# Kernel tuning notes

Measured on AMD Instinct MI355X. Metric: run time of the kernel, lower is better.

## Reference

```python
import jax, jax.numpy as jnp
import numpy as np

B, N, DIM = 1, 2048, 2048
H, KVH = 32, 4                 # query heads, kv heads
D = DIM // H                   # head_dim = 64
REP = H // KVH                 # queries per kv = 8
KV_DIM = D * KVH               # 256


def _rope_tables(n, d, base=10000.0):
    inv = 1.0 / (base ** (np.arange(0, d, 2, dtype=np.float32) / d))
    t = np.arange(n, dtype=np.float32)
    freqs = np.outer(t, inv)                      # [n, d/2]
    emb = np.concatenate([freqs, freqs], axis=-1)  # [n, d]
    return jnp.asarray(np.cos(emb)), jnp.asarray(np.sin(emb))


def setup_inputs() -> dict:
    key = jax.random.key(0)
    ks = jax.random.split(key, 5)
    s = 0.02
    cos, sin = _rope_tables(N, D)
    return {
        "x": jax.random.normal(ks[0], (B, N, DIM), jnp.float32),
        "Wq": jax.random.normal(ks[1], (DIM, DIM), jnp.float32) * s,
        "Wk": jax.random.normal(ks[2], (KV_DIM, DIM), jnp.float32) * s,
        "Wv": jax.random.normal(ks[3], (KV_DIM, DIM), jnp.float32) * s,
        "Wo": jax.random.normal(ks[4], (DIM, DIM), jnp.float32) * s,
        "cos": cos,
        "sin": sin,
    }


def _rotate_half(t):
    d2 = t.shape[-1] // 2
    return jnp.concatenate([-t[..., d2:], t[..., :d2]], axis=-1)


def reference(x, Wq, Wk, Wv, Wo, cos, sin):
    b, n, _ = x.shape
    # projections (nn.Linear: x @ W.T)
    q = (x @ Wq.T).reshape(b, n, H, D).transpose(0, 2, 1, 3)     # b h n d
    k = (x @ Wk.T).reshape(b, n, KVH, D).transpose(0, 2, 1, 3)   # b g n d
    v = (x @ Wv.T).reshape(b, n, KVH, D).transpose(0, 2, 1, 3)
    # RoPE
    c = cos[None, None, :, :]
    s = sin[None, None, :, :]
    q = q * c + _rotate_half(q) * s
    k = k * c + _rotate_half(k) * s
    # expand KV heads (repeat_interleave over head dim)
    k = jnp.repeat(k, REP, axis=1)   # b h n d
    v = jnp.repeat(v, REP, axis=1)
    # causal attention with materialized scores (faithful to source)
    scale = 1.0 / jnp.sqrt(jnp.asarray(D, x.dtype))
    scores = jnp.einsum('bhld,bhsd->bhls', q, k) * scale
    causal = jnp.tril(jnp.ones((n, n), bool))
    scores = jnp.where(causal[None, None], scores, jnp.asarray(-jnp.inf, x.dtype))
    attn = jax.nn.softmax(scores, axis=-1)
    y = jnp.einsum('bhls,bhsd->bhld', attn, v)       # b h n d
    y = y.transpose(0, 2, 1, 3).reshape(b, n, DIM)   # b n (h d)
    return y @ Wo.T
```

## Files before the change

kernel.cpp:

```cpp
#include <hip/hip_runtime.h>

typedef unsigned short u16;
typedef __attribute__((ext_vector_type(8))) short short8;
typedef __attribute__((ext_vector_type(4))) float floatx4;

#define N_TOK 2048
#define DIM   2048
#define NH    32
#define NKVH  4
#define HD    64
#define KVD   256

#define OFF_X   0
#define OFF_WQ  4194304
#define OFF_WK  8388608
#define OFF_WV  8912896
#define OFF_WO  9437184
#define OFF_QP  13631488
#define OFF_KP  17825792
#define OFF_VP  18350080
#define OFF_YB  18874368

__device__ __forceinline__ float bf2f(u16 u) {
  union { unsigned i; float f; } c; c.i = ((unsigned)u) << 16; return c.f;
}
__device__ __forceinline__ u16 f2bf(float f) {
  union { float f; unsigned i; } c; c.f = f;
  unsigned x = c.i;
  return (u16)((x + 0x7fffu + ((x >> 16) & 1u)) >> 16);
}

__device__ __forceinline__ void gload16(const u16* g, u16* l) {
#if defined(__has_builtin) && __has_builtin(__builtin_amdgcn_global_load_lds)
  __builtin_amdgcn_global_load_lds(
      (const __attribute__((address_space(1))) void*)g,
      (__attribute__((address_space(3))) void*)l, 16, 0, 0);
#else
  *(short8*)l = *(const short8*)g;
#endif
}


__global__ __launch_bounds__(256) void cvt_pack(const float* __restrict__ x,
                                                const float* __restrict__ wq,
                                                const float* __restrict__ wk,
                                                const float* __restrict__ wv,
                                                const float* __restrict__ wo,
                                                u16* __restrict__ ws) {
  __shared__ __align__(16) u16 Ls[2048];
  const int tid = threadIdx.x;
  const int rfg = blockIdx.x >> 4;
  const int kcg = blockIdx.x & 15;
  const float* src; u16* dst; int lrf;
  if      (rfg < 128) { src = x;  dst = ws + OFF_X;  lrf = rfg; }
  else if (rfg < 256) { src = wq; dst = ws + OFF_WQ; lrf = rfg - 128; }
  else if (rfg < 272) { src = wk; dst = ws + OFF_WK; lrf = rfg - 256; }
  else if (rfg < 288) { src = wv; dst = ws + OFF_WV; lrf = rfg - 272; }
  else                { src = wo; dst = ws + OFF_WO; lrf = rfg - 288; }

  const int rr = tid >> 4, cb = tid & 15;
  const float* s = src + (size_t)(lrf * 16 + rr) * DIM + kcg * 128 + cb * 8;
  float4 v0 = ((const float4*)s)[0];
  float4 v1 = ((const float4*)s)[1];
  ushort4 o0, o1;
  o0.x = f2bf(v0.x); o0.y = f2bf(v0.y); o0.z = f2bf(v0.z); o0.w = f2bf(v0.w);
  o1.x = f2bf(v1.x); o1.y = f2bf(v1.y); o1.z = f2bf(v1.z); o1.w = f2bf(v1.w);
  const int ch = cb >> 2, qq = cb & 3;
  u16* lp = &Ls[ch * 512 + (qq * 16 + rr) * 8];
  ((ushort4*)lp)[0] = o0;
  ((ushort4*)lp)[1] = o1;
  __syncthreads();
  const int och = tid >> 6, lane = tid & 63;
  *(short8*)(dst + ((size_t)(lrf * 64 + kcg * 4 + och)) * 512 + lane * 8) =
      *(const short8*)&Ls[och * 512 + lane * 8];
}


__global__ __launch_bounds__(256) void gemm_qkv(const u16* __restrict__ xp,
                                                const u16* __restrict__ Wqp,
                                                const u16* __restrict__ Wkp,
                                                const u16* __restrict__ Wvp,
                                                const float* __restrict__ cs,
                                                const float* __restrict__ sn,
                                                u16* __restrict__ Qp,
                                                u16* __restrict__ Kp,
                                                u16* __restrict__ Vp) {
  __shared__ __align__(16) u16 As[2][8 * 512];
  __shared__ __align__(16) u16 Bs[2][16 * 512];
  const int tid  = threadIdx.x;
  const int lane = tid & 63;
  const int w    = tid >> 6;
  const int r    = lane & 15, q = lane >> 4;
  const int tm = blockIdx.x & 31;
  const int tn = blockIdx.x >> 5;
  const int wm = w & 1, wn = w >> 1;

  const u16* Wp; int rfB0;
  if (tn < 16)      { Wp = Wqp; rfB0 = tn * 8; }
  else if (tn < 18) { Wp = Wkp; rfB0 = (tn - 16) * 8; }
  else              { Wp = Wvp; rfB0 = (tn - 18) * 8; }
  const int rfA0 = tm * 4;

  const int cA0 = w, cA1 = w + 4;
  const u16* aS0 = xp + ((size_t)(rfA0 + (cA0 >> 1)) * 64 + (cA0 & 1)) * 512 + lane * 8;
  const u16* aS1 = xp + ((size_t)(rfA0 + (cA1 >> 1)) * 64 + (cA1 & 1)) * 512 + lane * 8;
  const u16* bS[4];
#pragma unroll
  for (int j = 0; j < 4; ++j) {
    int ch = w + 4 * j;
    bS[j] = Wp + ((size_t)(rfB0 + (ch >> 1)) * 64 + (ch & 1)) * 512 + lane * 8;
  }

  floatx4 acc[2][4];
#pragma unroll
  for (int a = 0; a < 2; ++a)
#pragma unroll
    for (int b = 0; b < 4; ++b) acc[a][b] = (floatx4){0.f, 0.f, 0.f, 0.f};

  auto stage = [&](int b, int kt) {
    const size_t ko = (size_t)(kt * 2) * 512;
    gload16(aS0 + ko, &As[b][cA0 * 512 + lane * 8]);
    gload16(aS1 + ko, &As[b][cA1 * 512 + lane * 8]);
#pragma unroll
    for (int j = 0; j < 4; ++j)
      gload16(bS[j] + ko, &Bs[b][(w + 4 * j) * 512 + lane * 8]);
  };

  stage(0, 0);
  stage(1, 1);
  int cb = 0;
  for (int kt = 0; kt < 32; ++kt) {
    if (kt < 31) asm volatile("s_waitcnt vmcnt(6)" ::: "memory");
    else         asm volatile("s_waitcnt vmcnt(0)" ::: "memory");
    __builtin_amdgcn_s_barrier();
    __builtin_amdgcn_sched_barrier(0);

    short8 af[2][2], bf[4][2];
#pragma unroll
    for (int mi = 0; mi < 2; ++mi)
#pragma unroll
      for (int c = 0; c < 2; ++c)
        af[mi][c] = *(const short8*)&As[cb][((wm * 2 + mi) * 2 + c) * 512 + lane * 8];
#pragma unroll
    for (int nj = 0; nj < 4; ++nj)
#pragma unroll
      for (int c = 0; c < 2; ++c)
        bf[nj][c] = *(const short8*)&Bs[cb][((wn * 4 + nj) * 2 + c) * 512 + lane * 8];
#pragma unroll
    for (int c = 0; c < 2; ++c)
#pragma unroll
      for (int mi = 0; mi < 2; ++mi)
#pragma unroll
        for (int nj = 0; nj < 4; ++nj)
          acc[mi][nj] = __builtin_amdgcn_mfma_f32_16x16x32_bf16(af[mi][c], bf[nj][c], acc[mi][nj], 0, 0, 0);

    __builtin_amdgcn_sched_barrier(0);
    __builtin_amdgcn_s_barrier();
    if (kt + 2 < 32) stage(cb, kt + 2);
    cb ^= 1;
  }

  if (tn < 18) {
    const int head = (tn < 16) ? (tn * 2 + wn) : ((tn - 16) * 2 + wn);
#pragma unroll
    for (int mi = 0; mi < 2; ++mi)
#pragma unroll
      for (int g = 0; g < 4; ++g) {
        int row = tm * 64 + wm * 32 + mi * 16 + 4 * q + g;
        const float* crow  = cs + (size_t)row * 64;
        const float* srow2 = sn + (size_t)row * 64;
#pragma unroll
        for (int nj = 0; nj < 2; ++nj) {
          int d = nj * 16 + r;
          float x0 = acc[mi][nj][g];
          float x1 = acc[mi][nj + 2][g];
          float o0 = x0 * crow[d]      - x1 * srow2[d];
          float o1 = x1 * crow[d + 32] + x0 * srow2[d + 32];
          int qq = d >> 3, j = d & 7;
          int lslot = (qq * 16 + (row & 15)) * 8 + j;
          if (tn < 16) {
            int sq = row >> 5, ii = (row >> 4) & 1;
            size_t base = ((size_t)(head * 64 + sq) * 4 + ii * 2) * 512 + lslot;
            Qp[base]       = f2bf(o0);
            Qp[base + 512] = f2bf(o1);
          } else {
            int kt2 = row >> 6, t = (row >> 4) & 3;
            size_t base = ((size_t)(head * 32 + kt2) * 8 + t * 2) * 512 + lslot;
            Kp[base]       = f2bf(o0);
            Kp[base + 512] = f2bf(o1);
          }
        }
      }
  } else {
#pragma unroll
    for (int mi = 0; mi < 2; ++mi)
#pragma unroll
      for (int nj = 0; nj < 4; ++nj) {
        int col  = (tn - 18) * 128 + wn * 64 + nj * 16 + r;
        int kvh  = col >> 6;
        int t    = (col & 63) >> 4;
        int rr   = col & 15;
        int row0 = tm * 64 + wm * 32 + mi * 16 + 4 * q;
        int kt2  = row0 >> 6;
        int wk   = row0 & 63;
        int s    = wk >> 5;
        int qq   = (wk & 31) >> 3;
        int j0   = wk & 7;
        uint2 pk;
        pk.x = (unsigned)f2bf(acc[mi][nj][0]) | ((unsigned)f2bf(acc[mi][nj][1]) << 16);
        pk.y = (unsigned)f2bf(acc[mi][nj][2]) | ((unsigned)f2bf(acc[mi][nj][3]) << 16);
        size_t idx = ((size_t)(kvh * 32 + kt2) * 8 + s * 4 + t) * 512 + (qq * 16 + rr) * 8 + j0;
        *(uint2*)(Vp + idx) = pk;
      }
  }
}

__global__ __launch_bounds__(256) void gemm_out(const u16* __restrict__ Ap,
                                                const u16* __restrict__ Wp,
                                                float* __restrict__ C) {
  __shared__ __align__(16) u16 As[2][8 * 512];
  __shared__ __align__(16) u16 Bs[2][16 * 512];
  const int tid  = threadIdx.x;
  const int lane = tid & 63;
  const int w    = tid >> 6;
  const int r    = lane & 15, q = lane >> 4;
  const int tn = blockIdx.x & 15;
  const int tm = blockIdx.x >> 4;
  const int wm = w & 1, wn = w >> 1;

  const int rfA0 = tm * 4, rfB0 = tn * 8;
  const int cA0 = w, cA1 = w + 4;
  const u16* aS0 = Ap + ((size_t)(rfA0 + (cA0 >> 1)) * 64 + (cA0 & 1)) * 512 + lane * 8;
  const u16* aS1 = Ap + ((size_t)(rfA0 + (cA1 >> 1)) * 64 + (cA1 & 1)) * 512 + lane * 8;
  const u16* bS[4];
#pragma unroll
  for (int j = 0; j < 4; ++j) {
    int ch = w + 4 * j;
    bS[j] = Wp + ((size_t)(rfB0 + (ch >> 1)) * 64 + (ch & 1)) * 512 + lane * 8;
  }

  floatx4 acc[2][4];
#pragma unroll
  for (int a = 0; a < 2; ++a)
#pragma unroll
    for (int b = 0; b < 4; ++b) acc[a][b] = (floatx4){0.f, 0.f, 0.f, 0.f};

  auto stage = [&](int b, int kt) {
    const size_t ko = (size_t)(kt * 2) * 512;
    gload16(aS0 + ko, &As[b][cA0 * 512 + lane * 8]);
    gload16(aS1 + ko, &As[b][cA1 * 512 + lane * 8]);
#pragma unroll
    for (int j = 0; j < 4; ++j)
      gload16(bS[j] + ko, &Bs[b][(w + 4 * j) * 512 + lane * 8]);
  };

  stage(0, 0);
  stage(1, 1);
  int cb = 0;
  for (int kt = 0; kt < 32; ++kt) {
    if (kt < 31) asm volatile("s_waitcnt vmcnt(6)" ::: "memory");
    else         asm volatile("s_waitcnt vmcnt(0)" ::: "memory");
    __builtin_amdgcn_s_barrier();
    __builtin_amdgcn_sched_barrier(0);

    short8 af[2][2], bf[4][2];
#pragma unroll
    for (int mi = 0; mi < 2; ++mi)
#pragma unroll
      for (int c = 0; c < 2; ++c)
        af[mi][c] = *(const short8*)&As[cb][((wm * 2 + mi) * 2 + c) * 512 + lane * 8];
#pragma unroll
    for (int nj = 0; nj < 4; ++nj)
#pragma unroll
      for (int c = 0; c < 2; ++c)
        bf[nj][c] = *(const short8*)&Bs[cb][((wn * 4 + nj) * 2 + c) * 512 + lane * 8];
#pragma unroll
    for (int c = 0; c < 2; ++c)
#pragma unroll
      for (int mi = 0; mi < 2; ++mi)
#pragma unroll
        for (int nj = 0; nj < 4; ++nj)
          acc[mi][nj] = __builtin_amdgcn_mfma_f32_16x16x32_bf16(af[mi][c], bf[nj][c], acc[mi][nj], 0, 0, 0);

    __builtin_amdgcn_sched_barrier(0);
    __builtin_amdgcn_s_barrier();
    if (kt + 2 < 32) stage(cb, kt + 2);
    cb ^= 1;
  }

#pragma unroll
  for (int mi = 0; mi < 2; ++mi)
#pragma unroll
    for (int g = 0; g < 4; ++g) {
      int row = tm * 64 + wm * 32 + mi * 16 + 4 * q + g;
#pragma unroll
      for (int nj = 0; nj < 4; ++nj)
        C[(size_t)row * DIM + tn * 128 + wn * 64 + nj * 16 + r] = acc[mi][nj][g];
    }
}

__global__ __launch_bounds__(128, 2) void attn_mfma(const u16* __restrict__ Qp,
                                                    const u16* __restrict__ Kp,
                                                    const u16* __restrict__ Vp,
                                                    u16* __restrict__ Ybp) {
  __shared__ __align__(16) u16 Pl[2][32][72];
  __shared__ float OcA[32][66];
  __shared__ float OcB[32][66];
  __shared__ float LcA[2][64], LcB[2][64];
  const int tid  = threadIdx.x;
  const int lane = tid & 63;
  const int w    = tid >> 6;
  const int r    = lane & 15;
  const int q    = lane >> 4;
  const int p    = blockIdx.x;
  const int h    = blockIdx.y;
  const int kvh  = h >> 3;
  const int jA   = 63 - p;
  const int jB   = p;
  const int baseqA = jA * 32, baseqB = jB * 32;
  const int tA = (jA >> 1) + 1, tB = (jB >> 1) + 1;
  const int ktmaxA = tA - 1, ktmaxB = tB - 1;

  short8 qfA[2][2], qfB[2][2];
#pragma unroll
  for (int i = 0; i < 2; ++i)
#pragma unroll
    for (int c = 0; c < 2; ++c) {
      qfA[i][c] = *(const short8*)(Qp + ((size_t)(h * 64 + jA) * 4 + i * 2 + c) * 512 + lane * 8);
      qfB[i][c] = *(const short8*)(Qp + ((size_t)(h * 64 + jB) * 4 + i * 2 + c) * 512 + lane * 8);
    }

  floatx4 OA[2][4], OB[2][4];
  float lsumA[2], lsumB[2];
#pragma unroll
  for (int i = 0; i < 2; ++i) {
    lsumA[i] = 0.f; lsumB[i] = 0.f;
#pragma unroll
    for (int t = 0; t < 4; ++t) {
      OA[i][t] = (floatx4){0.f, 0.f, 0.f, 0.f};
      OB[i][t] = (floatx4){0.f, 0.f, 0.f, 0.f};
    }
  }

  const u16* Kbase = Kp + (size_t)(kvh * 32) * 8 * 512;
  const u16* Vbase = Vp + (size_t)(kvh * 32) * 8 * 512;

  auto loadK = [&](int kt, short8 (&kf)[4][2]) {
    const u16* kb = Kbase + (size_t)kt * 8 * 512 + lane * 8;
#pragma unroll
    for (int t = 0; t < 4; ++t) {
      kf[t][0] = *(const short8*)(kb + (t * 2 + 0) * 512);
      kf[t][1] = *(const short8*)(kb + (t * 2 + 1) * 512);
    }
  };

  auto body = [&](int kt, int ktmax, int baseq,
                  short8 (&qf)[2][2], floatx4 (&O)[2][4], float (&lsum)[2],
                  short8 (&kc)[4][2], short8 (&kn)[4][2]) {
    short8 vb[2][4];
    {
      const u16* vbp = Vbase + (size_t)kt * 8 * 512 + lane * 8;
#pragma unroll
      for (int s = 0; s < 2; ++s)
#pragma unroll
        for (int t = 0; t < 4; ++t)
          vb[s][t] = *(const short8*)(vbp + (s * 4 + t) * 512);
    }

    loadK(kt + 2 <= ktmax ? kt + 2 : ktmax, kn);

    floatx4 ST[2][4];
#pragma unroll
    for (int i = 0; i < 2; ++i)
#pragma unroll
      for (int t = 0; t < 4; ++t) ST[i][t] = (floatx4){0.f, 0.f, 0.f, 0.f};
#pragma unroll
    for (int t = 0; t < 4; ++t)
#pragma unroll
      for (int i = 0; i < 2; ++i) {
        ST[i][t] = __builtin_amdgcn_mfma_f32_16x16x32_bf16(kc[t][0], qf[i][0], ST[i][t], 0, 0, 0);
        ST[i][t] = __builtin_amdgcn_mfma_f32_16x16x32_bf16(kc[t][1], qf[i][1], ST[i][t], 0, 0, 0);
      }

    if (kt == ktmax) {
#pragma unroll
      for (int i = 0; i < 2; ++i) {
        int qrow = baseq + 16 * i + r;
#pragma unroll
        for (int t = 0; t < 4; ++t) {
          int key = kt * 64 + 16 * t + 4 * q;
#pragma unroll
          for (int g = 0; g < 4; ++g)
            if (key + g > qrow) ST[i][t][g] = -1e30f;
        }
      }
    }

#pragma unroll
    for (int i = 0; i < 2; ++i)
#pragma unroll
      for (int t = 0; t < 4; ++t) {
        float p0 = __expf(0.125f * ST[i][t][0]);
        float p1 = __expf(0.125f * ST[i][t][1]);
        float p2 = __expf(0.125f * ST[i][t][2]);
        float p3 = __expf(0.125f * ST[i][t][3]);
        lsum[i] += (p0 + p1) + (p2 + p3);
        uint2 pk;
        pk.x = (unsigned)f2bf(p0) | ((unsigned)f2bf(p1) << 16);
        pk.y = (unsigned)f2bf(p2) | ((unsigned)f2bf(p3) << 16);
        *(uint2*)&Pl[w][16 * i + r][16 * t + 4 * q] = pk;
      }

#pragma unroll
    for (int s = 0; s < 2; ++s)
#pragma unroll
      for (int i = 0; i < 2; ++i) {
        short8 pa = *(const short8*)&Pl[w][16 * i + r][32 * s + 8 * q];
#pragma unroll
        for (int t = 0; t < 4; ++t)
          O[i][t] = __builtin_amdgcn_mfma_f32_16x16x32_bf16(pa, vb[s][t], O[i][t], 0, 0, 0);
      }
  };

  auto runloop = [&](int start, int ktmax, int baseq,
                     short8 (&qf)[2][2], floatx4 (&O)[2][4], float (&lsum)[2]) {
    if (start > ktmax) return;
    short8 kA[4][2], kB[4][2];
    loadK(start, kA);
    for (int kt = start; kt <= ktmax; kt += 4) {
      body(kt, ktmax, baseq, qf, O, lsum, kA, kB);
      if (kt + 2 <= ktmax) body(kt + 2, ktmax, baseq, qf, O, lsum, kB, kA);
    }
  };

  runloop(w, ktmaxA, baseqA, qfA, OA, lsumA);
  const int sB = (w + tA) & 1;
  runloop(sB, ktmaxB, baseqB, qfB, OB, lsumB);

  if (w == 1) {
#pragma unroll
    for (int i = 0; i < 2; ++i) {
#pragma unroll
      for (int t = 0; t < 4; ++t)
#pragma unroll
        for (int g = 0; g < 4; ++g)
          OcA[(i * 4 + t) * 4 + g][lane] = OA[i][t][g];
      LcA[i][lane] = lsumA[i];
    }
  } else {
#pragma unroll
    for (int i = 0; i < 2; ++i) {
#pragma unroll
      for (int t = 0; t < 4; ++t)
#pragma unroll
        for (int g = 0; g < 4; ++g)
          OcB[(i * 4 + t) * 4 + g][lane] = OB[i][t][g];
      LcB[i][lane] = lsumB[i];
    }
  }
  __syncthreads();

  auto finalize = [&](int baseq, floatx4 (&O)[2][4], float (&lsum)[2]) {
#pragma unroll
    for (int i = 0; i < 2; ++i) {
      lsum[i] += __shfl_xor(lsum[i], 16);
      lsum[i] += __shfl_xor(lsum[i], 32);
    }
#pragma unroll
    for (int i = 0; i < 2; ++i) {
      float inv[4];
#pragma unroll
      for (int g = 0; g < 4; ++g)
        inv[g] = 1.f / __shfl(lsum[i], 4 * q + g);
#pragma unroll
      for (int g = 0; g < 4; ++g) {
        int rowi = baseq + 16 * i + 4 * q + g;
        size_t rbase = ((size_t)(rowi >> 4) * 64 + h * 2) * 512 +
                       (((r >> 3)) * 16 + (rowi & 15)) * 8 + (r & 7);
        Ybp[rbase]       = f2bf(O[i][0][g] * inv[g]);
        Ybp[rbase + 256] = f2bf(O[i][1][g] * inv[g]);
        Ybp[rbase + 512] = f2bf(O[i][2][g] * inv[g]);
        Ybp[rbase + 768] = f2bf(O[i][3][g] * inv[g]);
      }
    }
  };

  if (w == 0) {
#pragma unroll
    for (int i = 0; i < 2; ++i) {
#pragma unroll
      for (int t = 0; t < 4; ++t)
#pragma unroll
        for (int g = 0; g < 4; ++g)
          OA[i][t][g] += OcA[(i * 4 + t) * 4 + g][lane];
      lsumA[i] += LcA[i][lane];
    }
    finalize(baseqA, OA, lsumA);
  } else {
#pragma unroll
    for (int i = 0; i < 2; ++i) {
#pragma unroll
      for (int t = 0; t < 4; ++t)
#pragma unroll
        for (int g = 0; g < 4; ++g)
          OB[i][t][g] += OcB[(i * 4 + t) * 4 + g][lane];
      lsumB[i] += LcB[i][lane];
    }
    finalize(baseqB, OB, lsumB);
  }
}

extern "C" void kernel_launch(void* const* d_in, const int* in_sizes, int n_in,
                              void* d_out, int out_size, void* d_ws, size_t ws_size,
                              hipStream_t stream) {
  const float* x  = (const float*)d_in[0];
  const float* Wq = (const float*)d_in[1];
  const float* Wk = (const float*)d_in[2];
  const float* Wv = (const float*)d_in[3];
  const float* Wo = (const float*)d_in[4];
  const float* cs = (const float*)d_in[5];
  const float* sn = (const float*)d_in[6];

  u16* ws  = (u16*)d_ws;
  u16* xp  = ws + OFF_X;
  u16* Wqp = ws + OFF_WQ;
  u16* Wkp = ws + OFF_WK;
  u16* Wvp = ws + OFF_WV;
  u16* Wop = ws + OFF_WO;
  u16* Qp  = ws + OFF_QP;
  u16* Kp  = ws + OFF_KP;
  u16* Vp  = ws + OFF_VP;
  u16* Ybp = ws + OFF_YB;

  cvt_pack<<<dim3(6656), 256, 0, stream>>>(x, Wq, Wk, Wv, Wo, ws);

  gemm_qkv<<<dim3(640), 256, 0, stream>>>(xp, Wqp, Wkp, Wvp, cs, sn, Qp, Kp, Vp);

  attn_mfma<<<dim3(32, 32), 128, 0, stream>>>(Qp, Kp, Vp, Ybp);

  gemm_out<<<dim3(512), 256, 0, stream>>>(Ybp, Wop, (float*)d_out);
}
```

Measured before the change: 191.3 us.

## Split attention KV loop across four waves with staged LDS reduction

```diff
diff --git a/kernel.cpp b/kernel.cpp
--- a/kernel.cpp
+++ b/kernel.cpp
@@ -299,14 +299,13 @@
     }
 }
 
-__global__ __launch_bounds__(128, 2) void attn_mfma(const u16* __restrict__ Qp,
+__global__ __launch_bounds__(256, 4) void attn_mfma(const u16* __restrict__ Qp,
                                                     const u16* __restrict__ Kp,
                                                     const u16* __restrict__ Vp,
                                                     u16* __restrict__ Ybp) {
-  __shared__ __align__(16) u16 Pl[2][32][72];
-  __shared__ float OcA[32][66];
-  __shared__ float OcB[32][66];
-  __shared__ float LcA[2][64], LcB[2][64];
+  __shared__ __align__(16) u16 Pl[4][32][72];
+  __shared__ float Cb0[32][66], Cb1[32][66];
+  __shared__ float Lb0[2][64], Lb1[2][64];
   const int tid  = threadIdx.x;
   const int lane = tid & 63;
   const int w    = tid >> 6;
@@ -367,7 +366,7 @@
           vb[s][t] = *(const short8*)(vbp + (s * 4 + t) * 512);
     }
 
-    loadK(kt + 2 <= ktmax ? kt + 2 : ktmax, kn);
+    loadK(kt + 4 <= ktmax ? kt + 4 : ktmax, kn);
 
     floatx4 ST[2][4];
 #pragma unroll
@@ -427,37 +426,76 @@
     if (start > ktmax) return;
     short8 kA[4][2], kB[4][2];
     loadK(start, kA);
-    for (int kt = start; kt <= ktmax; kt += 4) {
+    for (int kt = start; kt <= ktmax; kt += 8) {
       body(kt, ktmax, baseq, qf, O, lsum, kA, kB);
-      if (kt + 2 <= ktmax) body(kt + 2, ktmax, baseq, qf, O, lsum, kB, kA);
+      if (kt + 4 <= ktmax) body(kt + 4, ktmax, baseq, qf, O, lsum, kB, kA);
     }
   };
 
   runloop(w, ktmaxA, baseqA, qfA, OA, lsumA);
-  const int sB = (w + tA) & 1;
+  const int sB = (w - tA) & 3;
   runloop(sB, ktmaxB, baseqB, qfB, OB, lsumB);
 
-  if (w == 1) {
+  auto pubA = [&] {
 #pragma unroll
     for (int i = 0; i < 2; ++i) {
 #pragma unroll
       for (int t = 0; t < 4; ++t)
 #pragma unroll
         for (int g = 0; g < 4; ++g)
-          OcA[(i * 4 + t) * 4 + g][lane] = OA[i][t][g];
-      LcA[i][lane] = lsumA[i];
-    }
-  } else {
+          Cb0[(i * 4 + t) * 4 + g][lane] = OA[i][t][g];
+      Lb0[i][lane] = lsumA[i];
+    }
+  };
+  auto pubB = [&] {
 #pragma unroll
     for (int i = 0; i < 2; ++i) {
 #pragma unroll
       for (int t = 0; t < 4; ++t)
 #pragma unroll
         for (int g = 0; g < 4; ++g)
-          OcB[(i * 4 + t) * 4 + g][lane] = OB[i][t][g];
-      LcB[i][lane] = lsumB[i];
-    }
-  }
+          Cb1[(i * 4 + t) * 4 + g][lane] = OB[i][t][g];
+      Lb1[i][lane] = lsumB[i];
+    }
+  };
+  auto addA = [&] {
+#pragma unroll
+    for (int i = 0; i < 2; ++i) {
+#pragma unroll
+      for (int t = 0; t < 4; ++t)
+#pragma unroll
+        for (int g = 0; g < 4; ++g)
+          OA[i][t][g] += Cb0[(i * 4 + t) * 4 + g][lane];
+      lsumA[i] += Lb0[i][lane];
+    }
+  };
+  auto addB = [&] {
+#pragma unroll
+    for (int i = 0; i < 2; ++i) {
+#pragma unroll
+      for (int t = 0; t < 4; ++t)
+#pragma unroll
+        for (int g = 0; g < 4; ++g)
+          OB[i][t][g] += Cb1[(i * 4 + t) * 4 + g][lane];
+      lsumB[i] += Lb1[i][lane];
+    }
+  };
+
+  if (w == 2) pubA;
+  if (w == 2) pubA();
+  if (w == 3) pubB();
+  __syncthreads();
+  if (w == 0) addA();
+  if (w == 1) addB();
+  __syncthreads();
+  if (w == 3) pubA();
+  if (w == 2) pubB();
+  __syncthreads();
+  if (w == 0) addA();
+  if (w == 1) addB();
+  __syncthreads();
+  if (w == 1) pubA();
+  if (w == 0) pubB();
   __syncthreads();
 
   auto finalize = [&](int baseq, floatx4 (&O)[2][4], float (&lsum)[2]) {
@@ -486,26 +524,10 @@
   };
 
   if (w == 0) {
-#pragma unroll
-    for (int i = 0; i < 2; ++i) {
-#pragma unroll
-      for (int t = 0; t < 4; ++t)
-#pragma unroll
-        for (int g = 0; g < 4; ++g)
-          OA[i][t][g] += OcA[(i * 4 + t) * 4 + g][lane];
-      lsumA[i] += LcA[i][lane];
-    }
+    addA();
     finalize(baseqA, OA, lsumA);
-  } else {
-#pragma unroll
-    for (int i = 0; i < 2; ++i) {
-#pragma unroll
-      for (int t = 0; t < 4; ++t)
-#pragma unroll
-        for (int g = 0; g < 4; ++g)
-          OB[i][t][g] += OcB[(i * 4 + t) * 4 + g][lane];
-      lsumB[i] += LcB[i][lane];
-    }
+  } else if (w == 1) {
+    addB();
     finalize(baseqB, OB, lsumB);
   }
 }
@@ -536,7 +558,7 @@
 
   gemm_qkv<<<dim3(640), 256, 0, stream>>>(xp, Wqp, Wkp, Wvp, cs, sn, Qp, Kp, Vp);
 
-  attn_mfma<<<dim3(32, 32), 128, 0, stream>>>(Qp, Kp, Vp, Ybp);
+  attn_mfma<<<dim3(32, 32), 256, 0, stream>>>(Qp, Kp, Vp, Ybp);
 
   gemm_out<<<dim3(512), 256, 0, stream>>>(Ybp, Wop, (float*)d_out);
 }
```

New measurement: 322.6 us. +68.6%, slower.
